# Performance work log

Hardware: AMD Instinct MI355X
Metric: run time of the kernel (lower is better)

The kernel has to match this reference:

```python
import jax, jax.numpy as jnp
import numpy as np

WINDOW_SIZE = 2
SOFTMAX_TEMP = 0.01
CART_RESOLUTION = 0.25
RANGE_KEEP = 3.0
EPS = 1e-12


def get_indices(batch_size, window_size):
    kp, dense = [], []
    for i in range(batch_size):
        for j in range(window_size - 1):
            kp.append(i * window_size + j)
            dense.append(i * window_size + j + 1)
    return np.asarray(kp), np.asarray(dense)


def normalize_coords(coords, height, width):
    # coords [B,N,2] pixel (u,v) -> [-1,1] (align_corners=True convention, as in the repo)
    u = 2.0 * coords[..., 0] / (width - 1) - 1.0
    v = 2.0 * coords[..., 1] / (height - 1) - 1.0
    return jnp.stack([u, v], axis=-1)


def grid_sample_bilinear(img, grid):
    # Matches torch F.grid_sample(mode='bilinear', padding_mode='zeros', align_corners=False)
    # img [B,C,H,W], grid [B,Hg,Wg,2] with (x,y) in [-1,1]
    B, C, H, W = img.shape
    x = ((grid[..., 0] + 1.0) * W - 1.0) * 0.5
    y = ((grid[..., 1] + 1.0) * H - 1.0) * 0.5
    x0 = jnp.floor(x); y0 = jnp.floor(y)
    wx1 = x - x0; wy1 = y - y0

    def gather(xi, yi):
        valid = (xi >= 0) & (xi <= W - 1) & (yi >= 0) & (yi <= H - 1)
        xc = jnp.clip(xi, 0, W - 1).astype(jnp.int32)
        yc = jnp.clip(yi, 0, H - 1).astype(jnp.int32)
        v = jax.vmap(lambda im, yy, xx: im[:, yy, xx])(img, yc, xc)  # [B,C,Hg,Wg]
        return v * valid[:, None].astype(img.dtype)

    x1 = x0 + 1.0; y1 = y0 + 1.0
    out = (gather(x0, y0) * ((1.0 - wx1) * (1.0 - wy1))[:, None]
           + gather(x1, y0) * (wx1 * (1.0 - wy1))[:, None]
           + gather(x0, y1) * ((1.0 - wx1) * wy1)[:, None]
           + gather(x1, y1) * (wx1 * wy1)[:, None])
    return out


def setup_inputs() -> dict:
    key = jax.random.key(0)
    k1, k2, k3, k4, k5 = jax.random.split(key, 5)
    BW, C, N, H, W = 4, 256, 1024, 256, 256
    return {
        "keypoint_scores": jax.random.uniform(k1, (BW, 1, N), jnp.float32),
        "keypoint_desc": jax.random.normal(k2, (BW, C, N), jnp.float32),
        "scores_dense": jax.random.uniform(k3, (BW, 1, H, W), jnp.float32),
        "desc_dense": jax.random.normal(k4, (BW, C, H, W), jnp.float32),
        "keypoint_coords": jax.random.uniform(k5, (BW, N, 2), jnp.float32) * (W - 1),
    }


def reference(keypoint_scores, keypoint_desc, scores_dense, desc_dense, keypoint_coords):
    BW, encoder_dim, n_points = keypoint_desc.shape
    batch_size = BW // WINDOW_SIZE
    _, _, height, width = desc_dense.shape
    kp_inds, dense_inds = get_indices(batch_size, WINDOW_SIZE)

    src_coords = keypoint_coords[kp_inds]                      # [B,N,2]
    src_desc = keypoint_desc[kp_inds]                          # [B,C,N]
    src_desc = src_desc / jnp.maximum(jnp.linalg.norm(src_desc, axis=1, keepdims=True), EPS)
    B = src_desc.shape[0]

    tgt_desc_dense = desc_dense[dense_inds]                    # [B,C,H,W]
    tgt = tgt_desc_dense.reshape(B, encoder_dim, height * width)
    tgt = tgt / jnp.maximum(jnp.linalg.norm(tgt, axis=1, keepdims=True), EPS)

    # dense correlation [B, n_points, H*W]
    match_vals = jnp.einsum('bcn,bcm->bnm', src_desc, tgt)

    # local window mask (vectorized equivalent of the B x n_points python loop)
    keep_range = int(RANGE_KEEP // CART_RESOLUTION + 1)
    uv = jax.lax.stop_gradient(jnp.trunc(src_coords)).astype(jnp.int32)  # [B,N,2]
    u = uv[..., 0][..., None]   # [B,N,1]
    v = uv[..., 1][..., None]
    vg = jnp.arange(height)[None, None, :]
    ug = jnp.arange(width)[None, None, :]
    vmask = (vg >= v - keep_range) & (vg <= v + keep_range)    # [B,N,H]
    umask = (ug >= u - keep_range) & (ug <= u + keep_range)    # [B,N,W]
    mask = (vmask[..., :, None] & umask[..., None, :]).reshape(B, n_points, height * width)
    match_vals = match_vals * mask.astype(match_vals.dtype)

    soft = jax.nn.softmax(match_vals / SOFTMAX_TEMP, axis=2)   # [B,N,HW]

    # soft-argmax over the dense grid (meshgrid 'ij': v over rows, u over cols)
    ucoord = jnp.tile(jnp.arange(width, dtype=jnp.float32), height)
    vcoord = jnp.repeat(jnp.arange(height, dtype=jnp.float32), width)
    coords = jnp.stack([ucoord, vcoord], axis=1)               # [HW,2]
    pseudo_coords = jnp.einsum('bnm,mc->bnc', soft, coords)    # [B,N,2]

    pseudo_norm = normalize_coords(pseudo_coords, height, width)[:, None]  # [B,1,N,2]

    tgt_scores_dense = scores_dense[dense_inds]                # [B,1,H,W]
    pseudo_scores = grid_sample_bilinear(tgt_scores_dense, pseudo_norm).reshape(B, 1, n_points)
    pseudo_desc = grid_sample_bilinear(tgt_desc_dense, pseudo_norm).reshape(B, encoder_dim, n_points)

    desc_match_score = jnp.sum(src_desc * pseudo_desc, axis=1, keepdims=True) / float(encoder_dim)
    src_scores = keypoint_scores[kp_inds]
    match_weights = 0.5 * (desc_match_score + 1.0) * src_scores * pseudo_scores  # score_comp=True

    return pseudo_coords, match_weights, jnp.asarray(kp_inds)
```

## Files before the change

kernel.cpp:

```cpp
#include <hip/hip_runtime.h>
#include <math.h>

#define HH 256
#define WW 256
#define CC 256
#define HW 65536
#define NPTS 1024
#define BB 2
#define KEEP 13
#define KEEPM 14
#define TINV 100.0f
#define EPSN 1e-12f
#define S_ALL 8355840.0f

#define TW 32
#define TH 4
#define TUN 8
#define TPB 512
#define NT  (BB * TPB)
#define CAPT 192
#define VSTRIDE 864
#define BPAD 36
#define KPB 64

__global__ __launch_bounds__(256) void prep_src(const float* __restrict__ kdesc,
                                                const float* __restrict__ kcoords,
                                                float* __restrict__ srcn,
                                                unsigned int* __restrict__ kparams) {
    __shared__ float tr[KPB][CC + 1];
    __shared__ float red[4][KPB];
    __shared__ float s_inv[KPB];
    int t = threadIdx.x;
    int kpt0 = blockIdx.x * KPB;
    int b = kpt0 >> 10;
    int n0 = kpt0 & 1023;
    const float* srcbase = kdesc + (size_t)(2 * b) * CC * NPTS;

    int cj = t >> 6, nj = t & 63;
    for (int c0 = 0; c0 < CC; c0 += 4)
        tr[nj][c0 + cj] = srcbase[(size_t)(c0 + cj) * NPTS + n0 + nj];
    __syncthreads();

    {
        int j = t & 63, p = t >> 6;
        float ss = 0.f;
#pragma unroll 8
        for (int i = 0; i < 64; i++) {
            float x = tr[j][p * 64 + i];
            ss = fmaf(x, x, ss);
        }
        red[p][j] = ss;
    }
    __syncthreads();
    if (t < KPB) {
        float ss = red[0][t] + red[1][t] + red[2][t] + red[3][t];
        s_inv[t] = 1.0f / fmaxf(sqrtf(ss), EPSN);
        int kpt = kpt0 + t;
        int n = kpt & 1023;
        float cu = kcoords[((size_t)(2 * b) * NPTS + n) * 2 + 0];
        float cv = kcoords[((size_t)(2 * b) * NPTS + n) * 2 + 1];
        int u = (int)truncf(cu), v = (int)truncf(cv);
        int u0m = max(0, u - KEEPM), u1m = min(WW - 1, u + KEEPM);
        int v0m = max(0, v - KEEPM), v1m = min(HH - 1, v + KEEPM);
        int nWm = u1m - u0m + 1, nHm = v1m - v0m + 1;
        kparams[kpt] = (unsigned)u0m | ((unsigned)v0m << 8) |
                       ((unsigned)nWm << 16) | ((unsigned)nHm << 24);
    }
    __syncthreads();
    for (int j = 0; j < KPB; j++)
        srcn[(size_t)(kpt0 + j) * CC + t] = tr[j][t] * s_inv[j];
}

__global__ __launch_bounds__(256) void corr_tiles(const float* __restrict__ ddense,
                                                  const float* __restrict__ srcn,
                                                  const unsigned int* __restrict__ kparams,
                                                  float* __restrict__ vals,
                                                  float* __restrict__ invn) {
    __shared__ __align__(16) float B_lds[CC][BPAD];
    __shared__ float s_inorm[TW * TH];
    __shared__ int s_kid[CAPT];
    __shared__ unsigned int s_kp[CAPT];
    __shared__ int s_cnt;

    int tileg = blockIdx.x;
    int b = tileg >> 9, tl = tileg & 511;
    int tv = tl >> 3, tu = tl & 7;
    int vb = tv * TH, ub = tu * TW;
    int t = threadIdx.x;
    if (t == 0) s_cnt = 0;
    __syncthreads();

    for (int i = t; i < NPTS; i += 256) {
        unsigned int kp = kparams[b * NPTS + i];
        int u0m = kp & 255, v0m = (kp >> 8) & 255;
        int nWm = (kp >> 16) & 255, nHm = (int)(kp >> 24);
        if (u0m <= ub + TW - 1 && u0m + nWm - 1 >= ub &&
            v0m <= vb + TH - 1 && v0m + nHm - 1 >= vb) {
            int slot = atomicAdd(&s_cnt, 1);
            if (slot < CAPT) {
                s_kid[slot] = b * NPTS + i;
                s_kp[slot] = kp;
            }
        }
    }
    __syncthreads();
    int nk = min(s_cnt, CAPT);
    if (nk == 0) return;

    int lane = t & 63;
    int half = lane >> 5;
    int pxg = lane & 31;
    int kg = t >> 6;
    int k8 = kg * 8;
    int px4 = pxg * 4;
    int wv = vb + (px4 >> 5), wu0 = ub + (px4 & 31);
    const float* abase = ddense + (size_t)(2 * b + 1) * CC * HW +
                         (size_t)half * HW + (size_t)wv * WW + wu0;

    for (int kc = 0; kc < nk; kc += 32) {
        int nkk = min(32, nk - kc);
#pragma unroll 4
        for (int i = 0; i < nkk; i++)
            B_lds[t][i] = srcn[(size_t)s_kid[kc + i] * CC + t];
        for (int i = nkk; i < 32; i++) B_lds[t][i] = 0.f;
        __syncthreads();

        float acc[4][8];
#pragma unroll
        for (int i = 0; i < 4; i++)
#pragma unroll
            for (int j = 0; j < 8; j++) acc[i][j] = 0.f;

        int kgn = (nkk + 7) >> 3;
        if (kg < kgn) {
            float ss0 = 0.f, ss1 = 0.f, ss2 = 0.f, ss3 = 0.f;
            bool dos = (kg == 0) && (kc == 0);
#pragma unroll 4
            for (int cc = 0; cc < CC / 2; cc++) {
                float4 av = *(const float4*)(abase + (size_t)cc * (2 * HW));
                const float* brow = &B_lds[2 * cc + half][k8];
                float b0 = brow[0], b1 = brow[1], b2 = brow[2], b3 = brow[3];
                float b4 = brow[4], b5 = brow[5], b6 = brow[6], b7 = brow[7];
                acc[0][0] = fmaf(av.x, b0, acc[0][0]);
                acc[0][1] = fmaf(av.x, b1, acc[0][1]);
                acc[0][2] = fmaf(av.x, b2, acc[0][2]);
                acc[0][3] = fmaf(av.x, b3, acc[0][3]);
                acc[0][4] = fmaf(av.x, b4, acc[0][4]);
                acc[0][5] = fmaf(av.x, b5, acc[0][5]);
                acc[0][6] = fmaf(av.x, b6, acc[0][6]);
                acc[0][7] = fmaf(av.x, b7, acc[0][7]);
                acc[1][0] = fmaf(av.y, b0, acc[1][0]);
                acc[1][1] = fmaf(av.y, b1, acc[1][1]);
                acc[1][2] = fmaf(av.y, b2, acc[1][2]);
                acc[1][3] = fmaf(av.y, b3, acc[1][3]);
                acc[1][4] = fmaf(av.y, b4, acc[1][4]);
                acc[1][5] = fmaf(av.y, b5, acc[1][5]);
                acc[1][6] = fmaf(av.y, b6, acc[1][6]);
                acc[1][7] = fmaf(av.y, b7, acc[1][7]);
                acc[2][0] = fmaf(av.z, b0, acc[2][0]);
                acc[2][1] = fmaf(av.z, b1, acc[2][1]);
                acc[2][2] = fmaf(av.z, b2, acc[2][2]);
                acc[2][3] = fmaf(av.z, b3, acc[2][3]);
                acc[2][4] = fmaf(av.z, b4, acc[2][4]);
                acc[2][5] = fmaf(av.z, b5, acc[2][5]);
                acc[2][6] = fmaf(av.z, b6, acc[2][6]);
                acc[2][7] = fmaf(av.z, b7, acc[2][7]);
                acc[3][0] = fmaf(av.w, b0, acc[3][0]);
                acc[3][1] = fmaf(av.w, b1, acc[3][1]);
                acc[3][2] = fmaf(av.w, b2, acc[3][2]);
                acc[3][3] = fmaf(av.w, b3, acc[3][3]);
                acc[3][4] = fmaf(av.w, b4, acc[3][4]);
                acc[3][5] = fmaf(av.w, b5, acc[3][5]);
                acc[3][6] = fmaf(av.w, b6, acc[3][6]);
                acc[3][7] = fmaf(av.w, b7, acc[3][7]);
                if (dos) {
                    ss0 = fmaf(av.x, av.x, ss0);
                    ss1 = fmaf(av.y, av.y, ss1);
                    ss2 = fmaf(av.z, av.z, ss2);
                    ss3 = fmaf(av.w, av.w, ss3);
                }
            }
#pragma unroll
            for (int i = 0; i < 4; i++)
#pragma unroll
                for (int j = 0; j < 8; j++)
                    acc[i][j] += __shfl_xor(acc[i][j], 32, 64);
            if (dos) {
                ss0 += __shfl_xor(ss0, 32, 64);
                ss1 += __shfl_xor(ss1, 32, 64);
                ss2 += __shfl_xor(ss2, 32, 64);
                ss3 += __shfl_xor(ss3, 32, 64);
                if (half == 0) {
                    float i0 = 1.0f / fmaxf(sqrtf(ss0), EPSN);
                    float i1 = 1.0f / fmaxf(sqrtf(ss1), EPSN);
                    float i2 = 1.0f / fmaxf(sqrtf(ss2), EPSN);
                    float i3 = 1.0f / fmaxf(sqrtf(ss3), EPSN);
                    s_inorm[px4 + 0] = i0;
                    s_inorm[px4 + 1] = i1;
                    s_inorm[px4 + 2] = i2;
                    s_inorm[px4 + 3] = i3;
                    float* ip = invn + (size_t)b * HW + wv * WW + wu0;
                    ip[0] = i0; ip[1] = i1; ip[2] = i2; ip[3] = i3;
                }
            }
        }
        if (kc == 0) __syncthreads();

        if (half == 0) {
            float iv0 = s_inorm[px4 + 0], iv1 = s_inorm[px4 + 1];
            float iv2 = s_inorm[px4 + 2], iv3 = s_inorm[px4 + 3];
#pragma unroll
            for (int j = 0; j < 8; j++) {
                int s = k8 + j;
                if (s < nkk) {
                    unsigned int kp = s_kp[kc + s];
                    int u0m = kp & 255, v0m = (kp >> 8) & 255;
                    int nWm = (kp >> 16) & 255, nHm = (int)(kp >> 24);
                    int dv = wv - v0m;
                    if ((unsigned)dv < (unsigned)nHm) {
                        int du0 = wu0 - u0m;
                        float* vp = vals + (size_t)s_kid[kc + s] * VSTRIDE +
                                    dv * nWm;
                        if ((unsigned)(du0 + 0) < (unsigned)nWm)
                            vp[du0 + 0] = acc[0][j] * iv0;
                        if ((unsigned)(du0 + 1) < (unsigned)nWm)
                            vp[du0 + 1] = acc[1][j] * iv1;
                        if ((unsigned)(du0 + 2) < (unsigned)nWm)
                            vp[du0 + 2] = acc[2][j] * iv2;
                        if ((unsigned)(du0 + 3) < (unsigned)nWm)
                            vp[du0 + 3] = acc[3][j] * iv3;
                    }
                }
            }
        }
        __syncthreads();
    }
}

__device__ inline float blockSum(float v, float* sred, int t) {
    for (int o = 32; o > 0; o >>= 1) v += __shfl_down(v, o, 64);
    __syncthreads();
    if ((t & 63) == 0) sred[t >> 6] = v;
    __syncthreads();
    return sred[0] + sred[1] + sred[2] + sred[3];
}

__global__ __launch_bounds__(256) void finish(const float* __restrict__ kscores,
                                              const float* __restrict__ sdense,
                                              const float* __restrict__ ddense,
                                              const float* __restrict__ kcoords,
                                              const float* __restrict__ srcn,
                                              const float* __restrict__ vals,
                                              const float* __restrict__ invn,
                                              float* __restrict__ out) {
    __shared__ float s_src[CC];
    __shared__ float s_red[4];
    int t = threadIdx.x;
    int kpt = blockIdx.x;
    int b = kpt >> 10, n = kpt & 1023;

    s_src[t] = srcn[(size_t)kpt * CC + t];

    float cu = kcoords[((size_t)(2 * b) * NPTS + n) * 2 + 0];
    float cv = kcoords[((size_t)(2 * b) * NPTS + n) * 2 + 1];
    int u = (int)truncf(cu), v = (int)truncf(cv);
    int u0 = max(0, u - KEEP), u1 = min(WW - 1, u + KEEP);
    int v0 = max(0, v - KEEP), v1 = min(HH - 1, v + KEEP);
    int nW = u1 - u0 + 1, nH = v1 - v0 + 1;
    int cnt = nW * nH;
    int u0m = max(0, u - KEEPM), u1m = min(WW - 1, u + KEEPM);
    int v0m = max(0, v - KEEPM), v1m = min(HH - 1, v + KEEPM);
    int nWm = u1m - u0m + 1, nHm = v1m - v0m + 1;
    int cntm = nWm * nHm;

    const float* vrow = vals + (size_t)kpt * VSTRIDE;
    __syncthreads();

    float valk[4];
    int puk[4], pvk[4];
    bool gk[4];
    float lm = -INFINITY;
#pragma unroll
    for (int k = 0; k < 4; k++) {
        int p = t + k * 256;
        bool gm = p < cntm;
        int pp = gm ? p : 0;
        int dvm = pp / nWm, dum = pp - dvm * nWm;
        int pu = u0m + dum, pv = v0m + dvm;
        bool inw = gm && pu >= u0 && pu <= u1 && pv >= v0 && pv <= v1;
        float val = inw ? vrow[pp] : 0.f;
        valk[k] = val;
        puk[k] = pu;
        pvk[k] = pv;
        gk[k] = inw;
        if (inw) lm = fmaxf(lm, val);
    }

    for (int o = 32; o > 0; o >>= 1) lm = fmaxf(lm, __shfl_down(lm, o, 64));
    if ((t & 63) == 0) s_red[t >> 6] = lm;
    __syncthreads();
    float m = fmaxf(fmaxf(s_red[0], s_red[1]), fmaxf(s_red[2], s_red[3]));
    m = fmaxf(m, 0.0f);

    float pse = 0.f, psu = 0.f, psv = 0.f;
#pragma unroll
    for (int k = 0; k < 4; k++) {
        float e = gk[k] ? expf(TINV * (valk[k] - m)) : 0.f;
        pse += e;
        psu = fmaf(e, (float)puk[k], psu);
        psv = fmaf(e, (float)pvk[k], psv);
    }
    float se = blockSum(pse, s_red, t);
    float su = blockSum(psu, s_red, t);
    float sv = blockSum(psv, s_red, t);

    float em = expf(-TINV * m);
    float sumWinU = 0.5f * (float)(u0 + u1) * (float)nW * (float)nH;
    float sumWinV = 0.5f * (float)(v0 + v1) * (float)nH * (float)nW;
    float denom = se + (65536.0f - (float)cnt) * em;
    float pcu = (su + em * (S_ALL - sumWinU)) / denom;
    float pcv = (sv + em * (S_ALL - sumWinV)) / denom;

    if (t == 0) {
        out[((size_t)b * NPTS + n) * 2 + 0] = pcu;
        out[((size_t)b * NPTS + n) * 2 + 1] = pcv;
    }

    float x = pcu * (256.0f / 255.0f) - 0.5f;
    float y = pcv * (256.0f / 255.0f) - 0.5f;
    float x0f = floorf(x), y0f = floorf(y);
    float wx = x - x0f, wy = y - y0f;
    int xi0 = (int)x0f, yi0 = (int)y0f, xi1 = xi0 + 1, yi1 = yi0 + 1;
    float w00 = (1.f - wx) * (1.f - wy), w10 = wx * (1.f - wy);
    float w01 = (1.f - wx) * wy, w11 = wx * wy;
    bool vx0 = (xi0 >= 0) & (xi0 < WW), vx1 = (xi1 >= 0) & (xi1 < WW);
    bool vy0 = (yi0 >= 0) & (yi0 < HH), vy1 = (yi1 >= 0) & (yi1 < HH);
    int cx0 = min(max(xi0, 0), WW - 1), cx1 = min(max(xi1, 0), WW - 1);
    int cy0 = min(max(yi0, 0), HH - 1), cy1 = min(max(yi1, 0), HH - 1);

    int cxs[4] = {cx0, cx1, cx0, cx1};
    int cys[4] = {cy0, cy0, cy1, cy1};
    bool cvalid[4] = {vx0 && vy0, vx1 && vy0, vx0 && vy1, vx1 && vy1};
    float wts[4] = {w00, w10, w01, w11};

    bool need = false;
    float dacc = 0.f;
#pragma unroll
    for (int c4 = 0; c4 < 4; c4++) {
        if (cvalid[c4]) {
            int du = cxs[c4] - u0m, dv = cys[c4] - v0m;
            if ((unsigned)du < (unsigned)nWm && (unsigned)dv < (unsigned)nHm) {
                float inv = invn[(size_t)b * HW + cys[c4] * WW + cxs[c4]];
                dacc = fmaf(wts[c4], vrow[dv * nWm + du] / inv, dacc);
            } else {
                need = true;
            }
        }
    }

    float dms;
    if (need) {
        const float* tgt = ddense + (size_t)(2 * b + 1) * CC * HW;
        int c = t;
        const float* ch = tgt + ((size_t)c << 16);
        float d00 = cvalid[0] ? ch[cys[0] * WW + cxs[0]] : 0.f;
        float d10 = cvalid[1] ? ch[cys[1] * WW + cxs[1]] : 0.f;
        float d01 = cvalid[2] ? ch[cys[2] * WW + cxs[2]] : 0.f;
        float d11 = cvalid[3] ? ch[cys[3] * WW + cxs[3]] : 0.f;
        float pd = d00 * wts[0] + d10 * wts[1] + d01 * wts[2] + d11 * wts[3];
        float dsum = blockSum(pd * s_src[c], s_red, t);
        dms = dsum / (float)CC;
    } else {
        dms = dacc / (float)CC;
    }

    if (t == 0) {
        const float* sch = sdense + (size_t)(2 * b + 1) * HW;
        float s00 = cvalid[0] ? sch[cys[0] * WW + cxs[0]] : 0.f;
        float s10 = cvalid[1] ? sch[cys[1] * WW + cxs[1]] : 0.f;
        float s01 = cvalid[2] ? sch[cys[2] * WW + cxs[2]] : 0.f;
        float s11 = cvalid[3] ? sch[cys[3] * WW + cxs[3]] : 0.f;
        float psc = s00 * wts[0] + s10 * wts[1] + s01 * wts[2] + s11 * wts[3];
        float sscore = kscores[(size_t)(2 * b) * NPTS + n];
        float wgt = 0.5f * (dms + 1.0f) * sscore * psc;
        out[2 * NPTS * BB + (size_t)b * NPTS + n] = wgt;
    }

    if (kpt == 0 && t < 2) out[3 * NPTS * BB + t] = 2.0f * (float)t;
}

__global__ __launch_bounds__(256) void prep_tgt(const float* __restrict__ dd,
                                                float* __restrict__ invn) {
    int idx = blockIdx.x * 256 + threadIdx.x;
    int b = idx >> 16, m = idx & 65535;
    const float* p = dd + (size_t)(2 * b + 1) * CC * HW + m;
    float ss = 0.f;
#pragma unroll 4
    for (int c = 0; c < CC; c++) {
        float x = p[(size_t)c << 16];
        ss += x * x;
    }
    invn[idx] = 1.0f / fmaxf(sqrtf(ss), EPSN);
}

__global__ __launch_bounds__(256) void matcher(const float* __restrict__ kscores,
                                               const float* __restrict__ sdense,
                                               const float* __restrict__ ddense,
                                               const float* __restrict__ kcoords,
                                               const float* __restrict__ srcn,
                                               const float* __restrict__ invn,
                                               float* __restrict__ out) {
    __shared__ float s_src[CC];
    __shared__ float s_red[4];
    int t = threadIdx.x;
    int kpt = blockIdx.x;
    int b = kpt >> 10, n = kpt & 1023;

    s_src[t] = srcn[(size_t)kpt * CC + t];

    float cu = kcoords[((size_t)(2 * b) * NPTS + n) * 2 + 0];
    float cv = kcoords[((size_t)(2 * b) * NPTS + n) * 2 + 1];
    int u = (int)truncf(cu), v = (int)truncf(cv);
    int u0 = max(0, u - KEEP), u1 = min(WW - 1, u + KEEP);
    int v0 = max(0, v - KEEP), v1 = min(HH - 1, v + KEEP);
    int nW = u1 - u0 + 1, nH = v1 - v0 + 1;
    int cnt = nW * nH;

    const float* tgt = ddense + (size_t)(2 * b + 1) * CC * HW;
    const float* inb = invn + (size_t)b * HW;
    __syncthreads();

    int p0 = t, p1 = t + 256, p2 = t + 512;
    bool g0 = p0 < cnt, g1 = p1 < cnt, g2 = p2 < cnt;
    int dv0 = p0 / nW, dv1 = p1 / nW, dv2 = p2 / nW;
    int uu0 = u0 + (p0 - dv0 * nW), uu1 = u0 + (p1 - dv1 * nW), uu2 = u0 + (p2 - dv2 * nW);
    int vv0 = v0 + dv0, vv1 = v0 + dv1, vv2 = v0 + dv2;
    int mi0 = g0 ? (vv0 * WW + uu0) : 0;
    int mi1 = g1 ? (vv1 * WW + uu1) : 0;
    int mi2 = g2 ? (vv2 * WW + uu2) : 0;

    const float* q0 = tgt + mi0;
    const float* q1 = tgt + mi1;
    const float* q2 = tgt + mi2;
    float a0 = 0.f, a1 = 0.f, a2 = 0.f;
#pragma unroll 4
    for (int c = 0; c < CC; c++) {
        float s = s_src[c];
        size_t off = (size_t)c << 16;
        a0 = fmaf(s, q0[off], a0);
        a1 = fmaf(s, q1[off], a1);
        a2 = fmaf(s, q2[off], a2);
    }
    float val0 = a0 * inb[mi0];
    float val1 = a1 * inb[mi1];
    float val2 = a2 * inb[mi2];

    float lm = fmaxf(fmaxf(g0 ? val0 : -INFINITY, g1 ? val1 : -INFINITY),
                     g2 ? val2 : -INFINITY);
    for (int o = 32; o > 0; o >>= 1) lm = fmaxf(lm, __shfl_down(lm, o, 64));
    if ((t & 63) == 0) s_red[t >> 6] = lm;
    __syncthreads();
    float m = fmaxf(fmaxf(s_red[0], s_red[1]), fmaxf(s_red[2], s_red[3]));
    m = fmaxf(m, 0.0f);

    float e0 = g0 ? expf(TINV * (val0 - m)) : 0.f;
    float e1 = g1 ? expf(TINV * (val1 - m)) : 0.f;
    float e2 = g2 ? expf(TINV * (val2 - m)) : 0.f;

    float se = blockSum(e0 + e1 + e2, s_red, t);
    float su = blockSum(e0 * uu0 + e1 * uu1 + e2 * uu2, s_red, t);
    float sv = blockSum(e0 * vv0 + e1 * vv1 + e2 * vv2, s_red, t);

    float em = expf(-TINV * m);
    float sumWinU = 0.5f * (float)(u0 + u1) * (float)nW * (float)nH;
    float sumWinV = 0.5f * (float)(v0 + v1) * (float)nH * (float)nW;
    float denom = se + (65536.0f - (float)cnt) * em;
    float pcu = (su + em * (S_ALL - sumWinU)) / denom;
    float pcv = (sv + em * (S_ALL - sumWinV)) / denom;

    if (t == 0) {
        out[((size_t)b * NPTS + n) * 2 + 0] = pcu;
        out[((size_t)b * NPTS + n) * 2 + 1] = pcv;
    }

    float x = pcu * (256.0f / 255.0f) - 0.5f;
    float y = pcv * (256.0f / 255.0f) - 0.5f;
    float x0f = floorf(x), y0f = floorf(y);
    float wx = x - x0f, wy = y - y0f;
    int xi0 = (int)x0f, yi0 = (int)y0f, xi1 = xi0 + 1, yi1 = yi0 + 1;
    float w00 = (1.f - wx) * (1.f - wy), w10 = wx * (1.f - wy);
    float w01 = (1.f - wx) * wy, w11 = wx * wy;
    bool vx0 = (xi0 >= 0) & (xi0 < WW), vx1 = (xi1 >= 0) & (xi1 < WW);
    bool vy0 = (yi0 >= 0) & (yi0 < HH), vy1 = (yi1 >= 0) & (yi1 < HH);
    int cx0 = min(max(xi0, 0), WW - 1), cx1 = min(max(xi1, 0), WW - 1);
    int cy0 = min(max(yi0, 0), HH - 1), cy1 = min(max(yi1, 0), HH - 1);

    {
        int c = t;
        const float* ch = tgt + ((size_t)c << 16);
        float d00 = (vx0 && vy0) ? ch[cy0 * WW + cx0] : 0.f;
        float d10 = (vx1 && vy0) ? ch[cy0 * WW + cx1] : 0.f;
        float d01 = (vx0 && vy1) ? ch[cy1 * WW + cx0] : 0.f;
        float d11 = (vx1 && vy1) ? ch[cy1 * WW + cx1] : 0.f;
        float pd = d00 * w00 + d10 * w10 + d01 * w01 + d11 * w11;
        float contrib = pd * s_src[c];
        float dsum = blockSum(contrib, s_red, t);
        if (t == 0) {
            float dms = dsum / (float)CC;
            const float* sch = sdense + (size_t)(2 * b + 1) * HW;
            float s00 = (vx0 && vy0) ? sch[cy0 * WW + cx0] : 0.f;
            float s10 = (vx1 && vy0) ? sch[cy0 * WW + cx1] : 0.f;
            float s01 = (vx0 && vy1) ? sch[cy1 * WW + cx0] : 0.f;
            float s11 = (vx1 && vy1) ? sch[cy1 * WW + cx1] : 0.f;
            float psc = s00 * w00 + s10 * w10 + s01 * w01 + s11 * w11;
            float sscore = kscores[(size_t)(2 * b) * NPTS + n];
            float wgt = 0.5f * (dms + 1.0f) * sscore * psc;
            out[2 * NPTS * BB + (size_t)b * NPTS + n] = wgt;
        }
    }

    if (kpt == 0 && t < 2) out[3 * NPTS * BB + t] = 2.0f * (float)t;
}

extern "C" void kernel_launch(void* const* d_in, const int* in_sizes, int n_in,
                              void* d_out, int out_size, void* d_ws, size_t ws_size,
                              hipStream_t stream) {
    const float* kscores = (const float*)d_in[0];
    const float* kdesc   = (const float*)d_in[1];
    const float* sdense  = (const float*)d_in[2];
    const float* ddense  = (const float*)d_in[3];
    const float* kcoords = (const float*)d_in[4];
    float* out = (float*)d_out;

    float* srcn = (float*)d_ws;
    float* vals = srcn + (size_t)BB * NPTS * CC;
    float* invn = vals + (size_t)BB * NPTS * VSTRIDE;
    unsigned int* kparams = (unsigned int*)(invn + (size_t)BB * HW);
    size_t need = ((size_t)BB * NPTS * CC + (size_t)BB * NPTS * VSTRIDE +
                   (size_t)BB * HW + BB * NPTS) * 4;

    if (ws_size >= need) {
        hipLaunchKernelGGL(prep_src, dim3(BB * NPTS / KPB), dim3(256), 0, stream,
                           kdesc, kcoords, srcn, kparams);
        hipLaunchKernelGGL(corr_tiles, dim3(NT), dim3(256), 0, stream,
                           ddense, srcn, kparams, vals, invn);
        hipLaunchKernelGGL(finish, dim3(BB * NPTS), dim3(256), 0, stream,
                           kscores, sdense, ddense, kcoords, srcn, vals, invn, out);
    } else {
        float* invn2 = srcn + (size_t)BB * NPTS * CC;
        hipLaunchKernelGGL(prep_src, dim3(BB * NPTS / KPB), dim3(256), 0, stream,
                           kdesc, kcoords, srcn, kparams);
        hipLaunchKernelGGL(prep_tgt, dim3(512), dim3(256), 0, stream, ddense, invn2);
        hipLaunchKernelGGL(matcher, dim3(BB * NPTS), dim3(256), 0, stream,
                           kscores, sdense, ddense, kcoords, srcn, invn2, out);
    }
}
```

Baseline: 81.24 us.

## Shrink correlation tiles to 16x4 and split channels four ways per wave

The corr_tiles kernel now uses 16x4 pixel tiles instead of 32x4, doubling the grid to 2048 blocks. Each wave splits the channel dimension into four quarters instead of two and reduces partial sums with an extra xor-16 shuffle. The goal is more parallelism, with fewer keypoints per tile so less wasted work on tiles that overlap few keypoint windows. In exchange, srcn rows are loaded into LDS by more blocks, loads per row are narrower (64B segments), and the shuffle reduction costs more.

```diff
diff --git a/kernel.cpp b/kernel.cpp
--- a/kernel.cpp
+++ b/kernel.cpp
@@ -13,11 +13,11 @@
 #define EPSN 1e-12f
 #define S_ALL 8355840.0f
 
-#define TW 32
-#define TH 4
-#define TUN 8
-#define TPB 512
-#define NT  (BB * TPB)
+#define CTW 16
+#define CTH 4
+#define CTUN 16
+#define CTPB 1024
+#define CNT (BB * CTPB)
 #define CAPT 192
 #define VSTRIDE 864
 #define BPAD 36
@@ -77,15 +77,15 @@
                                                   float* __restrict__ vals,
                                                   float* __restrict__ invn) {
     __shared__ __align__(16) float B_lds[CC][BPAD];
-    __shared__ float s_inorm[TW * TH];
+    __shared__ float s_inorm[CTW * CTH];
     __shared__ int s_kid[CAPT];
     __shared__ unsigned int s_kp[CAPT];
     __shared__ int s_cnt;
 
     int tileg = blockIdx.x;
-    int b = tileg >> 9, tl = tileg & 511;
-    int tv = tl >> 3, tu = tl & 7;
-    int vb = tv * TH, ub = tu * TW;
+    int b = tileg >> 10, tl = tileg & 1023;
+    int tv = tl >> 4, tu = tl & 15;
+    int vb = tv * CTH, ub = tu * CTW;
     int t = threadIdx.x;
     if (t == 0) s_cnt = 0;
     __syncthreads();
@@ -94,8 +94,8 @@
         unsigned int kp = kparams[b * NPTS + i];
         int u0m = kp & 255, v0m = (kp >> 8) & 255;
         int nWm = (kp >> 16) & 255, nHm = (int)(kp >> 24);
-        if (u0m <= ub + TW - 1 && u0m + nWm - 1 >= ub &&
-            v0m <= vb + TH - 1 && v0m + nHm - 1 >= vb) {
+        if (u0m <= ub + CTW - 1 && u0m + nWm - 1 >= ub &&
+            v0m <= vb + CTH - 1 && v0m + nHm - 1 >= vb) {
             int slot = atomicAdd(&s_cnt, 1);
             if (slot < CAPT) {
                 s_kid[slot] = b * NPTS + i;
@@ -108,14 +108,14 @@
     if (nk == 0) return;
 
     int lane = t & 63;
-    int half = lane >> 5;
-    int pxg = lane & 31;
+    int quarter = lane >> 4;
+    int pxg = lane & 15;
     int kg = t >> 6;
     int k8 = kg * 8;
     int px4 = pxg * 4;
-    int wv = vb + (px4 >> 5), wu0 = ub + (px4 & 31);
+    int wv = vb + (px4 >> 4), wu0 = ub + (px4 & 15);
     const float* abase = ddense + (size_t)(2 * b + 1) * CC * HW +
-                         (size_t)half * HW + (size_t)wv * WW + wu0;
+                         (size_t)quarter * HW + (size_t)wv * WW + wu0;
 
     for (int kc = 0; kc < nk; kc += 32) {
         int nkk = min(32, nk - kc);
@@ -136,9 +136,9 @@
             float ss0 = 0.f, ss1 = 0.f, ss2 = 0.f, ss3 = 0.f;
             bool dos = (kg == 0) && (kc == 0);
 #pragma unroll 4
-            for (int cc = 0; cc < CC / 2; cc++) {
-                float4 av = *(const float4*)(abase + (size_t)cc * (2 * HW));
-                const float* brow = &B_lds[2 * cc + half][k8];
+            for (int cc = 0; cc < CC / 4; cc++) {
+                float4 av = *(const float4*)(abase + (size_t)cc * (4 * HW));
+                const float* brow = &B_lds[4 * cc + quarter][k8];
                 float b0 = brow[0], b1 = brow[1], b2 = brow[2], b3 = brow[3];
                 float b4 = brow[4], b5 = brow[5], b6 = brow[6], b7 = brow[7];
                 acc[0][0] = fmaf(av.x, b0, acc[0][0]);
@@ -183,14 +183,20 @@
 #pragma unroll
             for (int i = 0; i < 4; i++)
 #pragma unroll
-                for (int j = 0; j < 8; j++)
+                for (int j = 0; j < 8; j++) {
+                    acc[i][j] += __shfl_xor(acc[i][j], 16, 64);
                     acc[i][j] += __shfl_xor(acc[i][j], 32, 64);
+                }
             if (dos) {
+                ss0 += __shfl_xor(ss0, 16, 64);
                 ss0 += __shfl_xor(ss0, 32, 64);
+                ss1 += __shfl_xor(ss1, 16, 64);
                 ss1 += __shfl_xor(ss1, 32, 64);
+                ss2 += __shfl_xor(ss2, 16, 64);
                 ss2 += __shfl_xor(ss2, 32, 64);
+                ss3 += __shfl_xor(ss3, 16, 64);
                 ss3 += __shfl_xor(ss3, 32, 64);
-                if (half == 0) {
+                if (quarter == 0) {
                     float i0 = 1.0f / fmaxf(sqrtf(ss0), EPSN);
                     float i1 = 1.0f / fmaxf(sqrtf(ss1), EPSN);
                     float i2 = 1.0f / fmaxf(sqrtf(ss2), EPSN);
@@ -206,7 +212,7 @@
         }
         if (kc == 0) __syncthreads();
 
-        if (half == 0) {
+        if (quarter == 0) {
             float iv0 = s_inorm[px4 + 0], iv1 = s_inorm[px4 + 1];
             float iv2 = s_inorm[px4 + 2], iv3 = s_inorm[px4 + 3];
 #pragma unroll
@@ -542,7 +548,7 @@
     if (ws_size >= need) {
         hipLaunchKernelGGL(prep_src, dim3(BB * NPTS / KPB), dim3(256), 0, stream,
                            kdesc, kcoords, srcn, kparams);
-        hipLaunchKernelGGL(corr_tiles, dim3(NT), dim3(256), 0, stream,
+        hipLaunchKernelGGL(corr_tiles, dim3(CNT), dim3(256), 0, stream,
                            ddense, srcn, kparams, vals, invn);
         hipLaunchKernelGGL(finish, dim3(BB * NPTS), dim3(256), 0, stream,
                            kscores, sdense, ddense, kcoords, srcn, vals, invn, out);
```

New measurement: 80.22 us. About the same (-1.3%).
